# Performance work log

Measured on AMD Instinct MI355X. Metric: run time of the kernel, lower is better.

Reference implementation:

```python
import jax, jax.numpy as jnp
import numpy as np

V, D, B, NEG = 100000, 128, 4096, 5
D_INNER = int(D * 2.0 * 2 / 3)  # nGPT FF inner dim = 170

def l2norm(t, axis=-1):
    return t / jnp.linalg.norm(t, axis=axis, keepdims=True)

def setup_inputs() -> dict:
    key = jax.random.key(0)
    ks = jax.random.split(key, 8)
    return {
        "input_ids": jax.random.randint(ks[0], (B,), 0, V),
        "target_ids": jax.random.randint(ks[1], (B,), 0, V),
        "neg_ids": jax.random.randint(ks[2], (B, NEG), 0, V),
        "W_in": jax.random.normal(ks[3], (V, D), jnp.float32) * (1.0 / np.sqrt(D)),
        "W_out": jax.random.normal(ks[4], (V, D), jnp.float32) * (1.0 / np.sqrt(D)),
        "W_hidden": jax.random.normal(ks[5], (D_INNER, D), jnp.float32) * 0.02,
        "W_gate": jax.random.normal(ks[6], (D_INNER, D), jnp.float32) * 0.02,
        "W_ff_out": jax.random.normal(ks[7], (D, D_INNER), jnp.float32) * 0.02,
        "hidden_scale": jnp.ones((D_INNER,), jnp.float32),
        "gate_scale": jnp.ones((D_INNER,), jnp.float32),
        "logit_scale": jnp.full((V,), D ** -0.5, dtype=jnp.float32),  # Scale param init = s_logit_scale
    }

def reference(input_ids, target_ids, neg_ids, W_in, W_out, W_hidden, W_gate,
              W_ff_out, hidden_scale, gate_scale, logit_scale):
    # skipgram: gather normalized input embeddings
    emb = l2norm(W_in)[input_ids]                                  # (B, D)
    # nGPT FeedForward: silu-gated, weights l2-normalized on input dim
    h = (emb @ l2norm(W_hidden).T) * hidden_scale                  # (B, D_INNER)
    g = (emb @ l2norm(W_gate).T) * gate_scale * jnp.sqrt(jnp.float32(D))
    x = jax.nn.silu(g) * h
    x = x @ l2norm(W_ff_out, axis=0).T                             # (B, D), to_out norm_dim_in=False
    # logits over full vocab, scaled by Scale(): param * (init/scale)
    scale_eff = logit_scale * (1.0 / (D ** -0.5))                  # (V,)
    logits = (x @ l2norm(W_out).T) * scale_eff                     # (B, V)
    # negative-sampling loss: gather positive + sampled negative logits
    pos = jnp.take_along_axis(logits, target_ids[:, None], axis=1)  # (B, 1)
    neg = jnp.take_along_axis(logits, neg_ids, axis=1)              # (B, NEG)
    positive_loss = jax.nn.log_sigmoid(pos).mean()
    negative_loss = jax.nn.log_sigmoid(-neg).mean()
    return -(positive_loss + negative_loss)
```

## Files before the change

kernel.cpp:

```cpp
#include <hip/hip_runtime.h>
#include <math.h>

#define DD    128
#define DI    170
#define DIP   176
#define ND4   32
#define ND4H  16
#define NI4P  44
#define BB    4096
#define NNEG  5
#define ROWS  4
#define NBLK  (BB / ROWS)
#define NTHR  512
#define NTASK (ROWS * (1 + NNEG))
#define SQRT_D 11.3137084989847603904f

#define WS_WHT 0
#define WS_WGT (ND4 * DIP * 4)
#define WS_WFT (2 * ND4 * DIP * 4)

__device__ __forceinline__ float wave_bcast_sum(float v) {
#pragma unroll
    for (int m = 1; m < 64; m <<= 1) v += __shfl_xor(v, m, 64);
    return v;
}

__global__ __launch_bounds__(256) void prep_kernel(
    const float* __restrict__ W_hidden,
    const float* __restrict__ W_gate,
    const float* __restrict__ W_ff_out,
    const float* __restrict__ hidden_scale,
    const float* __restrict__ gate_scale,
    float* __restrict__ ws,
    float* __restrict__ out)
{
    if (blockIdx.x == 0 && threadIdx.x == 0) out[0] = 0.0f;
    const int wave = threadIdx.x >> 6;
    const int lane = threadIdx.x & 63;
    const int t = blockIdx.x * 4 + wave;
    float* whT = ws + WS_WHT;
    float* wgT = ws + WS_WGT;
    float* wfT = ws + WS_WFT;

    if (t < DI) {
        const int v = t;
        float a = W_ff_out[(long)(2 * lane)     * DI + v];
        float b = W_ff_out[(long)(2 * lane + 1) * DI + v];
        float cf = wave_bcast_sum(a * a + b * b);
        float2 ph = ((const float2*)(W_hidden + (long)v * DD))[lane];
        float2 pg = ((const float2*)(W_gate   + (long)v * DD))[lane];
        float sh = wave_bcast_sum(ph.x * ph.x + ph.y * ph.y);
        float sg = wave_bcast_sum(pg.x * pg.x + pg.y * pg.y);
        const float whs = rsqrtf(sh) * hidden_scale[v] * rsqrtf(cf);
        const float wgs = rsqrtf(sg) * gate_scale[v] * SQRT_D;
        const int d4   = lane >> 1;
        const int half = lane & 1;
        float2* dh = (float2*)(whT + ((long)d4 * DIP + v) * 4 + half * 2);
        *dh = make_float2(ph.x * whs, ph.y * whs);
        float2* dg = (float2*)(wgT + ((long)d4 * DIP + v) * 4 + half * 2);
        *dg = make_float2(pg.x * wgs, pg.y * wgs);
    } else if (t < DI + NI4P) {
        const int i4 = t - DI;
#pragma unroll
        for (int rr = 0; rr < 2; ++rr) {
            const int dd = rr * 64 + lane;
            float4 v4;
            if (i4 < 42) {
                float2 lo = *(const float2*)(W_ff_out + (long)dd * DI + 4 * i4);
                float2 hi = *(const float2*)(W_ff_out + (long)dd * DI + 4 * i4 + 2);
                v4 = make_float4(lo.x, lo.y, hi.x, hi.y);
            } else if (i4 == 42) {
                float2 lo = *(const float2*)(W_ff_out + (long)dd * DI + 168);
                v4 = make_float4(lo.x, lo.y, 0.0f, 0.0f);
            } else {
                v4 = make_float4(0.0f, 0.0f, 0.0f, 0.0f);
            }
            *(float4*)(wfT + ((long)i4 * DD + dd) * 4) = v4;
        }
    } else if (t == DI + NI4P || t == DI + NI4P + 1) {
        float* base = (t == DI + NI4P) ? whT : wgT;
        for (int idx = lane; idx < ND4 * 6; idx += 64) {
            const int d4 = idx / 6, c = idx % 6;
            *(float4*)(base + ((long)d4 * DIP + DI + c) * 4) =
                make_float4(0.0f, 0.0f, 0.0f, 0.0f);
        }
    }
}

__global__ __launch_bounds__(NTHR, 8) void main_kernel(
    const int*   __restrict__ input_ids,
    const int*   __restrict__ target_ids,
    const int*   __restrict__ neg_ids,
    const float* __restrict__ W_in,
    const float* __restrict__ W_out,
    const float* __restrict__ logit_scale,
    const float* __restrict__ ws,
    float* __restrict__ out)
{
    __shared__ __align__(16) float s_emb[ROWS][DD];
    __shared__ __align__(16) float s_x[ROWS][DIP];
    __shared__ __align__(16) float s_pp[8][ROWS][DD];
    __shared__ __align__(16) float s_xout[ROWS][DD];
    __shared__ float s_part[DIP][9];
    __shared__ float s_red[8];

    const int tid  = threadIdx.x;
    const int wave = tid >> 6;
    const int lane = tid & 63;
    const int b0   = blockIdx.x * ROWS;

    const float4* whT4 = (const float4*)(ws + WS_WHT);
    const float4* wgT4 = (const float4*)(ws + WS_WGT);
    const float4* wfT4 = (const float4*)(ws + WS_WFT);

    if (wave < ROWS) {
        const int id = input_ids[b0 + wave];
        float2 p = ((const float2*)(W_in + (long)id * DD))[lane];
        float s  = wave_bcast_sum(p.x * p.x + p.y * p.y);
        float inv = rsqrtf(s);
        s_emb[wave][2 * lane]     = p.x * inv;
        s_emb[wave][2 * lane + 1] = p.y * inv;
    }
    __syncthreads();

    const bool gA = (tid < DIP);
    const bool gB = (tid >= 256 && tid < 256 + DIP);
    const int i = gA ? tid : (gB ? tid - 256 : -1);
    float ah[ROWS], ag[ROWS];
#pragma unroll
    for (int r = 0; r < ROWS; ++r) { ah[r] = 0.0f; ag[r] = 0.0f; }

    if (i >= 0) {
        const int d4lo = gA ? 0 : ND4H;
#pragma unroll 4
        for (int k = 0; k < ND4H; ++k) {
            const int d4 = d4lo + k;
            float4 h4 = whT4[d4 * DIP + i];
            float4 g4 = wgT4[d4 * DIP + i];
#pragma unroll
            for (int r = 0; r < ROWS; ++r) {
                float4 e4 = ((const float4*)s_emb[r])[d4];
                ah[r] += e4.x * h4.x + e4.y * h4.y + e4.z * h4.z + e4.w * h4.w;
                ag[r] += e4.x * g4.x + e4.y * g4.y + e4.z * g4.z + e4.w * g4.w;
            }
        }
    }
    if (gB) {
#pragma unroll
        for (int r = 0; r < ROWS; ++r) {
            s_part[i][r]        = ah[r];
            s_part[i][ROWS + r] = ag[r];
        }
    }
    __syncthreads();

    if (gA) {
#pragma unroll
        for (int r = 0; r < ROWS; ++r) {
            float h = ah[r] + s_part[i][r];
            float g = ag[r] + s_part[i][ROWS + r];
            float x = (g / (1.0f + __expf(-g))) * h;
            s_x[r][i] = x;
        }
    }
    __syncthreads();

    {
        const int i4lo = (wave < 4) ? 6 * wave : 24 + 5 * (wave - 4);
        const int i4n  = (wave < 4) ? 6 : 5;
        float acc0[ROWS], acc1[ROWS];
#pragma unroll
        for (int r = 0; r < ROWS; ++r) { acc0[r] = 0.0f; acc1[r] = 0.0f; }
        for (int k = 0; k < i4n; ++k) {
            const int i4 = i4lo + k;
            float4 wa = wfT4[i4 * DD + lane];
            float4 wb = wfT4[i4 * DD + 64 + lane];
#pragma unroll
            for (int r = 0; r < ROWS; ++r) {
                float4 x4 = ((const float4*)s_x[r])[i4];
                acc0[r] += wa.x * x4.x + wa.y * x4.y + wa.z * x4.z + wa.w * x4.w;
                acc1[r] += wb.x * x4.x + wb.y * x4.y + wb.z * x4.z + wb.w * x4.w;
            }
        }
#pragma unroll
        for (int r = 0; r < ROWS; ++r) {
            s_pp[wave][r][lane]      = acc0[r];
            s_pp[wave][r][64 + lane] = acc1[r];
        }
    }
    __syncthreads();

    {
        const int dd = tid & 127;
        const int r  = tid >> 7;
        float v = s_pp[0][r][dd];
#pragma unroll
        for (int q = 1; q < 8; ++q) v += s_pp[q][r][dd];
        s_xout[r][dd] = v;
    }
    __syncthreads();

    float wacc = 0.0f;
    for (int t = wave; t < NTASK; t += 8) {
        const int r  = t / (1 + NNEG);
        const int jj = t % (1 + NNEG);
        const int bidx = b0 + r;
        const int id = (jj == 0) ? target_ids[bidx] : neg_ids[bidx * NNEG + jj - 1];
        const float* wrow = W_out + (long)id * DD;
        float w0 = wrow[lane], w1 = wrow[64 + lane];
        float x0 = s_xout[r][lane], x1 = s_xout[r][64 + lane];
        float dot = w0 * x0 + w1 * x1;
        float ss  = w0 * w0 + w1 * w1;
#pragma unroll
        for (int m = 1; m < 64; m <<= 1) {
            dot += __shfl_xor(dot, m, 64);
            ss  += __shfl_xor(ss,  m, 64);
        }
        const float logit = dot * rsqrtf(ss) * logit_scale[id] * SQRT_D;
        const float z  = (jj == 0) ? logit : -logit;
        const float ls = fminf(z, 0.0f) - log1pf(__expf(-fabsf(z)));
        wacc += (jj == 0) ? ls * (1.0f / BB) : ls * (1.0f / (BB * NNEG));
    }
    if (lane == 0) s_red[wave] = wacc;
    __syncthreads();
    if (tid == 0) {
        float tot = s_red[0] + s_red[1] + s_red[2] + s_red[3]
                  + s_red[4] + s_red[5] + s_red[6] + s_red[7];
        atomicAdd(out, -tot);
    }
}

extern "C" void kernel_launch(void* const* d_in, const int* in_sizes, int n_in,
                              void* d_out, int out_size, void* d_ws, size_t ws_size,
                              hipStream_t stream) {
    (void)in_sizes; (void)n_in; (void)out_size; (void)ws_size;
    const int*   input_ids    = (const int*)  d_in[0];
    const int*   target_ids   = (const int*)  d_in[1];
    const int*   neg_ids      = (const int*)  d_in[2];
    const float* W_in         = (const float*)d_in[3];
    const float* W_out        = (const float*)d_in[4];
    const float* W_hidden     = (const float*)d_in[5];
    const float* W_gate       = (const float*)d_in[6];
    const float* W_ff_out     = (const float*)d_in[7];
    const float* hidden_scale = (const float*)d_in[8];
    const float* gate_scale   = (const float*)d_in[9];
    const float* logit_scale  = (const float*)d_in[10];
    float* out = (float*)d_out;
    float* ws  = (float*)d_ws;

    prep_kernel<<<54, 256, 0, stream>>>(W_hidden, W_gate, W_ff_out,
                                        hidden_scale, gate_scale, ws, out);
    main_kernel<<<NBLK, NTHR, 0, stream>>>(input_ids, target_ids, neg_ids,
                                           W_in, W_out, logit_scale, ws, out);
}
```

Baseline: 155.9 us.

## Process eight batch rows per block and rework the gathered-logit reduction

Doubles the rows handled per block from four to eight, so the normalized FF weights streamed from the workspace are reused across more rows and half as many blocks are launched. The gathered positive/negative logit computation is reorganized so eight threads per task load float4 chunks of the W_out row and reduce partial sums through shared memory, replacing the per-wave 64-lane shuffle reductions. In exchange the block uses more shared memory and registers, the launch bound drops to four blocks per CU, and one more barrier is added.

```diff
diff --git a/kernel.cpp b/kernel.cpp
--- a/kernel.cpp
+++ b/kernel.cpp
@@ -9,10 +9,11 @@
 #define NI4P  44
 #define BB    4096
 #define NNEG  5
-#define ROWS  4
+#define ROWS  8
 #define NBLK  (BB / ROWS)
 #define NTHR  512
 #define NTASK (ROWS * (1 + NNEG))
+#define XOP   132
 #define SQRT_D 11.3137084989847603904f
 
 #define WS_WHT 0
@@ -87,7 +88,7 @@
     }
 }
 
-__global__ __launch_bounds__(NTHR, 8) void main_kernel(
+__global__ __launch_bounds__(NTHR, 4) void main_kernel(
     const int*   __restrict__ input_ids,
     const int*   __restrict__ target_ids,
     const int*   __restrict__ neg_ids,
@@ -100,9 +101,12 @@
     __shared__ __align__(16) float s_emb[ROWS][DD];
     __shared__ __align__(16) float s_x[ROWS][DIP];
     __shared__ __align__(16) float s_pp[8][ROWS][DD];
-    __shared__ __align__(16) float s_xout[ROWS][DD];
-    __shared__ float s_part[DIP][9];
-    __shared__ float s_red[8];
+    __shared__ __align__(16) float s_xout[ROWS][XOP];
+    __shared__ float s_part[DIP][2 * ROWS + 1];
+    __shared__ float s_dp[NTASK][9];
+    __shared__ float s_sp[NTASK][9];
+    __shared__ float s_psc[NTASK];
+    __shared__ float s_ls[NTASK];
 
     const int tid  = threadIdx.x;
     const int wave = tid >> 6;
@@ -113,7 +117,7 @@
     const float4* wgT4 = (const float4*)(ws + WS_WGT);
     const float4* wfT4 = (const float4*)(ws + WS_WFT);
 
-    if (wave < ROWS) {
+    {
         const int id = input_ids[b0 + wave];
         float2 p = ((const float2*)(W_in + (long)id * DD))[lane];
         float s  = wave_bcast_sum(p.x * p.x + p.y * p.y);
@@ -192,40 +196,58 @@
 
     {
         const int dd = tid & 127;
-        const int r  = tid >> 7;
-        float v = s_pp[0][r][dd];
-#pragma unroll
-        for (int q = 1; q < 8; ++q) v += s_pp[q][r][dd];
-        s_xout[r][dd] = v;
-    }
-    __syncthreads();
-
-    float wacc = 0.0f;
-    for (int t = wave; t < NTASK; t += 8) {
+        const int r0 = tid >> 7;
+#pragma unroll
+        for (int rr = 0; rr < 2; ++rr) {
+            const int r = r0 + 4 * rr;
+            float v = s_pp[0][r][dd];
+#pragma unroll
+            for (int q = 1; q < 8; ++q) v += s_pp[q][r][dd];
+            s_xout[r][dd] = v;
+        }
+    }
+    __syncthreads();
+
+    if (tid < NTASK * 8) {
+        const int t  = tid >> 3;
+        const int c  = tid & 7;
         const int r  = t / (1 + NNEG);
         const int jj = t % (1 + NNEG);
         const int bidx = b0 + r;
         const int id = (jj == 0) ? target_ids[bidx] : neg_ids[bidx * NNEG + jj - 1];
-        const float* wrow = W_out + (long)id * DD;
-        float w0 = wrow[lane], w1 = wrow[64 + lane];
-        float x0 = s_xout[r][lane], x1 = s_xout[r][64 + lane];
-        float dot = w0 * x0 + w1 * x1;
-        float ss  = w0 * w0 + w1 * w1;
-#pragma unroll
-        for (int m = 1; m < 64; m <<= 1) {
-            dot += __shfl_xor(dot, m, 64);
-            ss  += __shfl_xor(ss,  m, 64);
-        }
-        const float logit = dot * rsqrtf(ss) * logit_scale[id] * SQRT_D;
+        if (c == 0) s_psc[t] = logit_scale[id];
+        const float4* wrow4 = (const float4*)(W_out + (long)id * DD);
+        const float4* xr4   = (const float4*)&s_xout[r][0];
+        float dot = 0.0f, ss = 0.0f;
+#pragma unroll
+        for (int k2 = 0; k2 < 4; ++k2) {
+            const int j = c + 8 * k2;
+            float4 w4 = wrow4[j];
+            float4 x4 = xr4[j];
+            dot += w4.x * x4.x + w4.y * x4.y + w4.z * x4.z + w4.w * x4.w;
+            ss  += w4.x * w4.x + w4.y * w4.y + w4.z * w4.z + w4.w * w4.w;
+        }
+        s_dp[t][c] = dot;
+        s_sp[t][c] = ss;
+    }
+    __syncthreads();
+
+    if (tid < NTASK) {
+        const int t  = tid;
+        const int jj = t % (1 + NNEG);
+        float dot = s_dp[t][0], ss = s_sp[t][0];
+#pragma unroll
+        for (int c = 1; c < 8; ++c) { dot += s_dp[t][c]; ss += s_sp[t][c]; }
+        const float logit = dot * rsqrtf(ss) * s_psc[t] * SQRT_D;
         const float z  = (jj == 0) ? logit : -logit;
         const float ls = fminf(z, 0.0f) - log1pf(__expf(-fabsf(z)));
-        wacc += (jj == 0) ? ls * (1.0f / BB) : ls * (1.0f / (BB * NNEG));
-    }
-    if (lane == 0) s_red[wave] = wacc;
+        s_ls[t] = (jj == 0) ? ls * (1.0f / BB) : ls * (1.0f / (BB * NNEG));
+    }
     __syncthreads();
     if (tid == 0) {
-        float tot = s_red[0] + s_red[1] + s_red[2] + s_red[3]
-                  + s_red[4] + s_red[5] + s_red[6] + s_red[7];
+        float tot = 0.0f;
+#pragma unroll
+        for (int t = 0; t < NTASK; ++t) tot += s_ls[t];
         atomicAdd(out, -tot);
     }
 }
```

After: 148.5 us. 1.05x faster.
